# Optimization experiments

Measured on AMD Instinct MI355X. Metric: run time of the kernel, lower is better.

The kernel has to match this reference:

```python
import jax, jax.numpy as jnp
import numpy as np

N_NODES = 50000
N_EDGES = 800000
N_IN = 128
N_OPEN = 64
N_OUT = 40
N_LAYER = 4


def setup_inputs() -> dict:
    key = jax.random.key(0)
    ks = jax.random.split(key, 8)
    stdv, stdvp = 0.01, 1e-4
    KN1 = jnp.tile(jnp.eye(N_OPEN, dtype=jnp.float32)[None], (N_LAYER, 1, 1)) \
        + jax.random.uniform(ks[3], (N_LAYER, N_OPEN, N_OPEN), jnp.float32) * stdvp
    return {
        "xn": jax.random.normal(ks[0], (1, N_IN, N_NODES), jnp.float32),
        "K1Nopen": jax.random.normal(ks[1], (N_OPEN, N_IN), jnp.float32) * stdv,
        "KNclose": jax.random.normal(ks[2], (N_OUT, N_OPEN), jnp.float32) * stdv,
        "KN1": KN1,
        "att_src": 0.001 * jnp.ones((N_LAYER, 1, N_OPEN), jnp.float32),
        "att_dst": 0.001 * jnp.ones((N_LAYER, 1, N_OPEN), jnp.float32),
        "omega": jnp.ones((N_LAYER, N_OPEN), jnp.float32),
        "edge_i": jax.random.randint(ks[4], (N_EDGES,), 0, N_NODES, jnp.int32),
        "edge_j": jax.random.randint(ks[5], (N_EDGES,), 0, N_NODES, jnp.int32),
    }


def segment_softmax(logits, seg, num_segments):
    # numerically-stable softmax grouped by destination node (torch_geometric.utils.softmax)
    m = jax.ops.segment_max(logits, seg, num_segments=num_segments)
    e = jnp.exp(logits - m[seg])
    d = jax.ops.segment_sum(e, seg, num_segments=num_segments)
    return e / d[seg]


def reference(xn, K1Nopen, KNclose, KN1, att_src, att_dst, omega, edge_i, edge_j):
    N = xn.shape[-1]
    # gcn_norm(add_self_loops=True): augment edge list with self loops
    loops = jnp.arange(N, dtype=edge_i.dtype)
    I = jnp.concatenate([edge_i, loops])
    J = jnp.concatenate([edge_j, loops])

    # opening layer: 1x1 conv == matmul over channels, then relu
    x = jax.nn.relu(jnp.einsum('oc,bcn->bon', K1Nopen, xn))  # (1, nopen, N)

    for i in range(KN1.shape[0]):
        feat = x[0]  # (C, N), H=1 head
        # per-edge attention logits: a_src . x[:, I] + a_dst . x[:, J]
        a = att_src[i, 0] @ feat[:, I] + att_dst[i, 0] @ feat[:, J]  # (E,)
        a = jax.nn.leaky_relu(a, 0.2)
        W = segment_softmax(a, I, N)  # softmax over incoming edges of each node I
        # neighborNode: weighted gather of source features; neighborEdge: scatter-sum to dst
        msg = W[None, :] * feat[:, J]  # (C, E)
        spatial = jax.ops.segment_sum(msg.T, I, num_segments=N).T[None]  # (1, C, N)
        # omega residual mixing (per-channel)
        x = x - omega[i][None, :, None] * (x - spatial)
        # singleLayer openclose, act=False inside, relu outside
        x = jax.nn.relu(jnp.einsum('oc,bcn->bon', KN1[i], x))

    x = jnp.einsum('oc,bcn->bon', KNclose, x)  # (1, num_output, N)
    out = jax.nn.log_softmax(x[0].T, axis=-1)  # (N, num_output)
    return out
```

## Files before the change

### kernel.cpp

```cpp
#include <hip/hip_runtime.h>

#define NN 50000
#define NE 800000
#define NET 850000
#define OPEN_BLOCKS 782
#define EPB 1087
#define CAP 96

typedef unsigned int uint;
typedef unsigned short ushort;
typedef __attribute__((ext_vector_type(8))) short short8v;
typedef __attribute__((ext_vector_type(4))) float f32x4;

__device__ __forceinline__ float bcast_lane(float v, int l) {
    return __int_as_float(__builtin_amdgcn_readlane(__float_as_int(v), l));
}
__device__ __forceinline__ int ibcast(int v, int l) {
    return __builtin_amdgcn_readlane(v, l);
}
__device__ __forceinline__ float wred_max(float v) {
#pragma unroll
    for (int off = 32; off; off >>= 1) v = fmaxf(v, __shfl_xor(v, off, 64));
    return v;
}
__device__ __forceinline__ float wred_sum(float v) {
#pragma unroll
    for (int off = 32; off; off >>= 1) v += __shfl_xor(v, off, 64);
    return v;
}
__device__ __forceinline__ void wred_max2(float& a, float& b) {
#pragma unroll
    for (int off = 32; off; off >>= 1) {
        float ta = __shfl_xor(a, off, 64);
        float tb = __shfl_xor(b, off, 64);
        a = fmaxf(a, ta);
        b = fmaxf(b, tb);
    }
}
__device__ __forceinline__ void wred_sum2(float& a, float& b) {
#pragma unroll
    for (int off = 32; off; off >>= 1) {
        float ta = __shfl_xor(a, off, 64);
        float tb = __shfl_xor(b, off, 64);
        a += ta;
        b += tb;
    }
}
__device__ __forceinline__ ushort f2bf(float f) {
    uint u = __float_as_uint(f);
    return (ushort)((u + 0x7fffu + ((u >> 16) & 1u)) >> 16);
}
__device__ __forceinline__ float bflo(uint u) { return __uint_as_float(u << 16); }
__device__ __forceinline__ float bfhi(uint u) { return __uint_as_float(u & 0xffff0000u); }
__device__ __forceinline__ float lrelu(float a) { return (a > 0.f) ? a : 0.2f * a; }

__device__ __forceinline__ void acc8_fma(float* acc8, float wgt, uint4 v) {
    acc8[0] = fmaf(wgt, bflo(v.x), acc8[0]);
    acc8[1] = fmaf(wgt, bfhi(v.x), acc8[1]);
    acc8[2] = fmaf(wgt, bflo(v.y), acc8[2]);
    acc8[3] = fmaf(wgt, bfhi(v.y), acc8[3]);
    acc8[4] = fmaf(wgt, bflo(v.z), acc8[4]);
    acc8[5] = fmaf(wgt, bfhi(v.z), acc8[5]);
    acc8[6] = fmaf(wgt, bflo(v.w), acc8[6]);
    acc8[7] = fmaf(wgt, bfhi(v.w), acc8[7]);
}
__device__ __forceinline__ uint4 pack8(const float* v) {
    uint4 p;
    p.x = (uint)f2bf(v[0]) | ((uint)f2bf(v[1]) << 16);
    p.y = (uint)f2bf(v[2]) | ((uint)f2bf(v[3]) << 16);
    p.z = (uint)f2bf(v[4]) | ((uint)f2bf(v[5]) << 16);
    p.w = (uint)f2bf(v[6]) | ((uint)f2bf(v[7]) << 16);
    return p;
}

__device__ void node_aggregate_generic(const ushort* __restrict__ xin,
                                       const float* __restrict__ darr,
                                       const int* __restrict__ csrj,
                                       int rs, int deg, float s_n,
                                       int lane, int c8, float* out8) {
    float acc8[8] = {0.f, 0.f, 0.f, 0.f, 0.f, 0.f, 0.f, 0.f};
    int re = rs + deg;
    float mxd = -1e30f;
    for (int e = rs + lane; e < re; e += 64) mxd = fmaxf(mxd, darr[csrj[e]]);
    mxd = wred_max(mxd);
    float mx = lrelu(s_n + mxd);
    float sm = 0.f;
    for (int e = rs + lane; e < re; e += 64)
        sm += __expf(lrelu(s_n + darr[csrj[e]]) - mx);
    sm = wred_sum(sm);
    float inv = 1.f / sm;
    for (int e = rs; e < re; ++e) {
        int j = csrj[e];
        float w = __expf(lrelu(s_n + darr[j]) - mx);
        uint4 v = *(const uint4*)(xin + (((size_t)j) << 6) + (c8 << 3));
        acc8_fma(acc8, w, v);
    }
#pragma unroll
    for (int q = 0; q < 8; ++q) out8[q] = acc8[q] * inv;
}

__device__ __forceinline__ void dual_aggregate(const ushort* __restrict__ xin,
                                               const float* __restrict__ darr,
                                               const int* __restrict__ csrj,
                                               int r0, int deg0, float sn0, int jl0, float dl0,
                                               int r1, int deg1, float sn1, int jl1, float dl1,
                                               int lane, int g, int c8,
                                               float* o0, float* o1) {
    if (deg0 <= 64 && deg1 <= 64) {
        float m0 = dl0, m1 = dl1;
        wred_max2(m0, m1);
        float mx0 = lrelu(sn0 + m0);
        float mx1 = lrelu(sn1 + m1);
        float w0 = (lane < deg0) ? __expf(lrelu(sn0 + dl0) - mx0) : 0.f;
        float w1 = (lane < deg1) ? __expf(lrelu(sn1 + dl1) - mx1) : 0.f;
        float su0 = w0, su1 = w1;
        wred_sum2(su0, su1);
        float inv0 = 1.f / su0, inv1 = 1.f / su1;

        float acc0[8] = {0.f, 0.f, 0.f, 0.f, 0.f, 0.f, 0.f, 0.f};
        float acc1[8] = {0.f, 0.f, 0.f, 0.f, 0.f, 0.f, 0.f, 0.f};
        int md = min(deg0, deg1);
        int tt = 0;
        for (; tt + 16 <= md; tt += 16) {
            int e0 = tt + g, e1 = tt + 8 + g;
            int   ja = __shfl(jl0, e0); float wa = __shfl(w0, e0);
            int   jb = __shfl(jl0, e1); float wb = __shfl(w0, e1);
            int   jc = __shfl(jl1, e0); float wc = __shfl(w1, e0);
            int   jd = __shfl(jl1, e1); float wd = __shfl(w1, e1);
            uint4 va = *(const uint4*)(xin + (((size_t)ja) << 6) + (c8 << 3));
            uint4 vb = *(const uint4*)(xin + (((size_t)jb) << 6) + (c8 << 3));
            uint4 vc = *(const uint4*)(xin + (((size_t)jc) << 6) + (c8 << 3));
            uint4 vd = *(const uint4*)(xin + (((size_t)jd) << 6) + (c8 << 3));
            acc8_fma(acc0, wa, va);
            acc8_fma(acc0, wb, vb);
            acc8_fma(acc1, wc, vc);
            acc8_fma(acc1, wd, vd);
        }
        for (; tt + 8 <= md; tt += 8) {
            int e = tt + g;
            int   ja = __shfl(jl0, e); float wa = __shfl(w0, e);
            int   jc = __shfl(jl1, e); float wc = __shfl(w1, e);
            uint4 va = *(const uint4*)(xin + (((size_t)ja) << 6) + (c8 << 3));
            uint4 vc = *(const uint4*)(xin + (((size_t)jc) << 6) + (c8 << 3));
            acc8_fma(acc0, wa, va);
            acc8_fma(acc1, wc, vc);
        }
        for (int u = tt; u < deg0; u += 8) {
            int e = u + g;
            bool ok = e < deg0;
            int ec = ok ? e : 0;
            int   j = __shfl(jl0, ec);
            float w = ok ? __shfl(w0, ec) : 0.f;
            uint4 v = *(const uint4*)(xin + (((size_t)j) << 6) + (c8 << 3));
            acc8_fma(acc0, w, v);
        }
        for (int u = tt; u < deg1; u += 8) {
            int e = u + g;
            bool ok = e < deg1;
            int ec = ok ? e : 0;
            int   j = __shfl(jl1, ec);
            float w = ok ? __shfl(w1, ec) : 0.f;
            uint4 v = *(const uint4*)(xin + (((size_t)j) << 6) + (c8 << 3));
            acc8_fma(acc1, w, v);
        }
#pragma unroll
        for (int q = 0; q < 8; ++q) {
            float a = acc0[q], b = acc1[q];
            float ta = __shfl_xor(a, 8, 64),  tb = __shfl_xor(b, 8, 64);
            a += ta; b += tb;
            ta = __shfl_xor(a, 16, 64); tb = __shfl_xor(b, 16, 64);
            a += ta; b += tb;
            ta = __shfl_xor(a, 32, 64); tb = __shfl_xor(b, 32, 64);
            a += ta; b += tb;
            o0[q] = a * inv0;
            o1[q] = b * inv1;
        }
    } else {
        node_aggregate_generic(xin, darr, csrj, r0, deg0, sn0, lane, c8, o0);
        node_aggregate_generic(xin, darr, csrj, r1, deg1, sn1, lane, c8, o1);
    }
}

__device__ __forceinline__ void fill_edge(int* __restrict__ deg,
                                          int* __restrict__ csrj, int i, int j,
                                          int& slot_out, bool ok) {
    slot_out = ok ? atomicAdd(&deg[i], 1) : 0;
}

__device__ __forceinline__ void fill_phase(const int* __restrict__ ei,
                                           const int* __restrict__ ej,
                                           int* __restrict__ deg,
                                           int* __restrict__ csrj,
                                           int bid, int t) {
    int base = bid * EPB;
    int end = base + EPB;
    if (end > NET) end = NET;
    int e0 = base + t, e1 = e0 + 256, e2 = e0 + 512, e3 = e0 + 768, e4 = e0 + 1024;
    bool o0 = e0 < end, o1 = e1 < end, o2 = e2 < end, o3 = e3 < end, o4 = e4 < end;
    int i0 = 0, j0 = 0, i1 = 0, j1 = 0, i2 = 0, j2 = 0, i3 = 0, j3 = 0, i4 = 0, j4 = 0;
    if (o0) { if (e0 < NE) { i0 = ei[e0]; j0 = ej[e0]; } else { i0 = e0 - NE; j0 = i0; } }
    if (o1) { if (e1 < NE) { i1 = ei[e1]; j1 = ej[e1]; } else { i1 = e1 - NE; j1 = i1; } }
    if (o2) { if (e2 < NE) { i2 = ei[e2]; j2 = ej[e2]; } else { i2 = e2 - NE; j2 = i2; } }
    if (o3) { if (e3 < NE) { i3 = ei[e3]; j3 = ej[e3]; } else { i3 = e3 - NE; j3 = i3; } }
    if (o4) { if (e4 < NE) { i4 = ei[e4]; j4 = ej[e4]; } else { i4 = e4 - NE; j4 = i4; } }
    int p0 = 0, p1 = 0, p2 = 0, p3 = 0, p4 = 0;
    if (o0) p0 = atomicAdd(&deg[i0], 1);
    if (o1) p1 = atomicAdd(&deg[i1], 1);
    if (o2) p2 = atomicAdd(&deg[i2], 1);
    if (o3) p3 = atomicAdd(&deg[i3], 1);
    if (o4) p4 = atomicAdd(&deg[i4], 1);
    if (o0 && p0 < CAP) csrj[(size_t)i0 * CAP + p0] = j0;
    if (o1 && p1 < CAP) csrj[(size_t)i1 * CAP + p1] = j1;
    if (o2 && p2 < CAP) csrj[(size_t)i2 * CAP + p2] = j2;
    if (o3 && p3 < CAP) csrj[(size_t)i3 * CAP + p3] = j3;
    if (o4 && p4 < CAP) csrj[(size_t)i4 * CAP + p4] = j4;
}

__global__ __launch_bounds__(256) void k_openfill(const float* __restrict__ xn,
                                                  const float* __restrict__ K1,
                                                  const float* __restrict__ att_s,
                                                  const float* __restrict__ att_d,
                                                  ushort* __restrict__ x0,
                                                  float* __restrict__ s0,
                                                  float* __restrict__ d0,
                                                  const int* __restrict__ ei,
                                                  const int* __restrict__ ej,
                                                  int* __restrict__ deg,
                                                  int* __restrict__ csrj) {
    __shared__ float xs[64][65];
    __shared__ float Kt[64][65];
    int t = threadIdx.x;
    int bid = blockIdx.x;

    bool fill_first = (bid & 1);
    if (fill_first) fill_phase(ei, ej, deg, csrj, bid, t);

    int n0 = bid * 64;
    int tx = t & 15;
    int ty = t >> 4;
    float acc[4][4] = {};

    for (int half = 0; half < 2; ++half) {
        if (half) __syncthreads();
        for (int idx = t; idx < 4096; idx += 256) {
            int c = idx >> 6, o = idx & 63;
            Kt[c][o] = K1[o * 128 + half * 64 + c];
        }
        if (n0 + 64 <= NN) {
            for (int idx = t; idx < 1024; idx += 256) {
                int c = idx >> 4, l4 = (idx & 15) * 4;
                float4 v = *(const float4*)&xn[(size_t)(half * 64 + c) * NN + n0 + l4];
                *(float4*)&xs[c][l4] = v;
            }
        } else {
            for (int idx = t; idx < 4096; idx += 256) {
                int c = idx >> 6, ln = idx & 63;
                int n = n0 + ln;
                xs[c][ln] = (n < NN) ? xn[(size_t)(half * 64 + c) * NN + n] : 0.f;
            }
        }
        __syncthreads();

        for (int c = 0; c < 64; ++c) {
            float4 xv = *(const float4*)&xs[c][ty * 4];
            float4 kv = *(const float4*)&Kt[c][tx * 4];
            acc[0][0] = fmaf(xv.x, kv.x, acc[0][0]); acc[0][1] = fmaf(xv.x, kv.y, acc[0][1]);
            acc[0][2] = fmaf(xv.x, kv.z, acc[0][2]); acc[0][3] = fmaf(xv.x, kv.w, acc[0][3]);
            acc[1][0] = fmaf(xv.y, kv.x, acc[1][0]); acc[1][1] = fmaf(xv.y, kv.y, acc[1][1]);
            acc[1][2] = fmaf(xv.y, kv.z, acc[1][2]); acc[1][3] = fmaf(xv.y, kv.w, acc[1][3]);
            acc[2][0] = fmaf(xv.z, kv.x, acc[2][0]); acc[2][1] = fmaf(xv.z, kv.y, acc[2][1]);
            acc[2][2] = fmaf(xv.z, kv.z, acc[2][2]); acc[2][3] = fmaf(xv.z, kv.w, acc[2][3]);
            acc[3][0] = fmaf(xv.w, kv.x, acc[3][0]); acc[3][1] = fmaf(xv.w, kv.y, acc[3][1]);
            acc[3][2] = fmaf(xv.w, kv.z, acc[3][2]); acc[3][3] = fmaf(xv.w, kv.w, acc[3][3]);
        }
    }

    float asv[4], adv[4];
#pragma unroll
    for (int j = 0; j < 4; ++j) { asv[j] = att_s[tx * 4 + j]; adv[j] = att_d[tx * 4 + j]; }

#pragma unroll
    for (int i = 0; i < 4; ++i) {
        int n = n0 + ty * 4 + i;
        if (n < NN) {
            float4 r;
            r.x = fmaxf(acc[i][0], 0.f); r.y = fmaxf(acc[i][1], 0.f);
            r.z = fmaxf(acc[i][2], 0.f); r.w = fmaxf(acc[i][3], 0.f);
            float ps = r.x * asv[0] + r.y * asv[1] + r.z * asv[2] + r.w * asv[3];
            float pd = r.x * adv[0] + r.y * adv[1] + r.z * adv[2] + r.w * adv[3];
#pragma unroll
            for (int off = 1; off < 16; off <<= 1) {
                ps += __shfl_xor(ps, off, 64);
                pd += __shfl_xor(pd, off, 64);
            }
            if (tx == 0) { s0[n] = ps; d0[n] = pd; }
            ushort4 h;
            h.x = f2bf(r.x); h.y = f2bf(r.y); h.z = f2bf(r.z); h.w = f2bf(r.w);
            *(ushort4*)&x0[(size_t)n * 64 + tx * 4] = h;
        }
    }

    if (!fill_first) fill_phase(ei, ej, deg, csrj, bid, t);
}

template <int SD>
__global__ __launch_bounds__(256, 4) void k_layer(const ushort* __restrict__ xin,
                                                  ushort* __restrict__ xout,
                                                  const float* __restrict__ sarr,
                                                  const float* __restrict__ darr,
                                                  float* __restrict__ snext,
                                                  float* __restrict__ dnext,
                                                  const int* __restrict__ deg,
                                                  const int* __restrict__ csrj,
                                                  const float* __restrict__ Kl,
                                                  const float* __restrict__ om_l,
                                                  const float* __restrict__ atts_n,
                                                  const float* __restrict__ attd_n) {
    __shared__ ushort Tl[32][72];
    __shared__ ushort Kb[64][72];
    __shared__ float spart[32], dpart[32];

    int t = threadIdx.x;
    int lane = t & 63;
    int wid = t >> 6;
    int g = lane >> 3, c8 = lane & 7;

    for (int u = t; u < 512; u += 256) {
        int row = u >> 3, cb = (u & 7) * 8;
        float4 f0 = *(const float4*)&Kl[row * 64 + cb];
        float4 f1 = *(const float4*)&Kl[row * 64 + cb + 4];
        float v8[8] = {f0.x, f0.y, f0.z, f0.w, f1.x, f1.y, f1.z, f1.w};
        *(uint4*)&Kb[row][cb] = pack8(v8);
    }
    if (SD && t < 32) { spart[t] = 0.f; dpart[t] = 0.f; }

    float om8[8];
    {
        float4 a = *(const float4*)&om_l[c8 * 8];
        float4 b = *(const float4*)&om_l[c8 * 8 + 4];
        om8[0] = a.x; om8[1] = a.y; om8[2] = a.z; om8[3] = a.w;
        om8[4] = b.x; om8[5] = b.y; om8[6] = b.z; om8[7] = b.w;
    }

    int nblk = blockIdx.x * 32;
    int nw0 = nblk + wid * 8;

    int   dgv = ((lane < 8) && (nw0 + lane < NN)) ? deg[nw0 + lane] : 0;
    float snv = ((lane < 8) && (nw0 + lane < NN)) ? sarr[nw0 + lane] : 0.f;

    const uint4 zero4 = {0u, 0u, 0u, 0u};

    bool  c_v = (nw0 < NN);
    int   c_deg0 = min(ibcast(dgv, 0), CAP);
    int   c_deg1 = min(ibcast(dgv, 1), CAP);
    int   c_b0 = nw0 * CAP, c_b1 = (nw0 + 1) * CAP;
    float c_sn0 = bcast_lane(snv, 0), c_sn1 = bcast_lane(snv, 1);
    int   c_jl0 = (lane < c_deg0) ? csrj[c_b0 + lane] : 0;
    int   c_jl1 = (lane < c_deg1) ? csrj[c_b1 + lane] : 0;
    float c_dl0 = (lane < c_deg0) ? darr[c_jl0] : -1e30f;
    float c_dl1 = (lane < c_deg1) ? darr[c_jl1] : -1e30f;
    uint4 c_x0 = c_v ? *(const uint4*)(xin + (((size_t)nw0) << 6) + (c8 << 3)) : zero4;
    uint4 c_x1 = c_v ? *(const uint4*)(xin + (((size_t)(nw0 + 1)) << 6) + (c8 << 3)) : zero4;

#pragma unroll
    for (int rp = 0; rp < 4; ++rp) {
        int   nx_b0 = 0, nx_b1 = 0, nx_deg0 = 0, nx_deg1 = 0, nx_jl0 = 0, nx_jl1 = 0;
        float nx_sn0 = 0.f, nx_sn1 = 0.f, nx_dl0 = -1e30f, nx_dl1 = -1e30f;
        uint4 nx_x0 = zero4, nx_x1 = zero4;
        bool  nx_v = false;
        if (rp < 3) {
            int nn0 = nw0 + 2 * rp + 2;
            nx_v = (nn0 < NN);
            nx_deg0 = min(ibcast(dgv, 2 * rp + 2), CAP);
            nx_deg1 = min(ibcast(dgv, 2 * rp + 3), CAP);
            nx_b0 = nn0 * CAP;
            nx_b1 = (nn0 + 1) * CAP;
            nx_sn0 = bcast_lane(snv, 2 * rp + 2);
            nx_sn1 = bcast_lane(snv, 2 * rp + 3);
            nx_jl0 = (lane < nx_deg0) ? csrj[nx_b0 + lane] : 0;
            nx_jl1 = (lane < nx_deg1) ? csrj[nx_b1 + lane] : 0;
            nx_dl0 = (lane < nx_deg0) ? darr[nx_jl0] : -1e30f;
            nx_dl1 = (lane < nx_deg1) ? darr[nx_jl1] : -1e30f;
            if (nx_v) {
                nx_x0 = *(const uint4*)(xin + (((size_t)nn0) << 6) + (c8 << 3));
                nx_x1 = *(const uint4*)(xin + (((size_t)(nn0 + 1)) << 6) + (c8 << 3));
            }
        }

        if (c_v) {
            float t0a[8], t1a[8];
            dual_aggregate(xin, darr, csrj, c_b0, c_deg0, c_sn0, c_jl0, c_dl0,
                           c_b1, c_deg1, c_sn1, c_jl1, c_dl1, lane, g, c8, t0a, t1a);

            float xc;
            xc = bflo(c_x0.x); t0a[0] = xc - om8[0] * (xc - t0a[0]);
            xc = bfhi(c_x0.x); t0a[1] = xc - om8[1] * (xc - t0a[1]);
            xc = bflo(c_x0.y); t0a[2] = xc - om8[2] * (xc - t0a[2]);
            xc = bfhi(c_x0.y); t0a[3] = xc - om8[3] * (xc - t0a[3]);
            xc = bflo(c_x0.z); t0a[4] = xc - om8[4] * (xc - t0a[4]);
            xc = bfhi(c_x0.z); t0a[5] = xc - om8[5] * (xc - t0a[5]);
            xc = bflo(c_x0.w); t0a[6] = xc - om8[6] * (xc - t0a[6]);
            xc = bfhi(c_x0.w); t0a[7] = xc - om8[7] * (xc - t0a[7]);
            xc = bflo(c_x1.x); t1a[0] = xc - om8[0] * (xc - t1a[0]);
            xc = bfhi(c_x1.x); t1a[1] = xc - om8[1] * (xc - t1a[1]);
            xc = bflo(c_x1.y); t1a[2] = xc - om8[2] * (xc - t1a[2]);
            xc = bfhi(c_x1.y); t1a[3] = xc - om8[3] * (xc - t1a[3]);
            xc = bflo(c_x1.z); t1a[4] = xc - om8[4] * (xc - t1a[4]);
            xc = bfhi(c_x1.z); t1a[5] = xc - om8[5] * (xc - t1a[5]);
            xc = bflo(c_x1.w); t1a[6] = xc - om8[6] * (xc - t1a[6]);
            xc = bfhi(c_x1.w); t1a[7] = xc - om8[7] * (xc - t1a[7]);

            int lr = wid * 8 + 2 * rp;
            if (g == 0) {
                *(uint4*)&Tl[lr][c8 * 8] = pack8(t0a);
            } else if (g == 1) {
                *(uint4*)&Tl[lr + 1][c8 * 8] = pack8(t1a);
            }
        }

        c_b0 = nx_b0; c_b1 = nx_b1; c_v = nx_v;
        c_deg0 = nx_deg0; c_deg1 = nx_deg1;
        c_sn0 = nx_sn0; c_sn1 = nx_sn1;
        c_jl0 = nx_jl0; c_jl1 = nx_jl1;
        c_dl0 = nx_dl0; c_dl1 = nx_dl1;
        c_x0 = nx_x0; c_x1 = nx_x1;
    }
    __syncthreads();

    {
        int mt = wid >> 1;
        int arow = mt * 16 + (lane & 15);
        int koff = (lane >> 4) * 8;
        short8v a0 = *(const short8v*)&Tl[arow][koff];
        short8v a1 = *(const short8v*)&Tl[arow][32 + koff];
        int col0 = (wid & 1) * 32 + (lane & 15);
        int col1 = col0 + 16;
        short8v b00 = *(const short8v*)&Kb[col0][koff];
        short8v b01 = *(const short8v*)&Kb[col0][32 + koff];
        short8v b10 = *(const short8v*)&Kb[col1][koff];
        short8v b11 = *(const short8v*)&Kb[col1][32 + koff];
        f32x4 acc0 = {0.f, 0.f, 0.f, 0.f};
        f32x4 acc1 = {0.f, 0.f, 0.f, 0.f};
        acc0 = __builtin_amdgcn_mfma_f32_16x16x32_bf16(a0, b00, acc0, 0, 0, 0);
        acc0 = __builtin_amdgcn_mfma_f32_16x16x32_bf16(a1, b01, acc0, 0, 0, 0);
        acc1 = __builtin_amdgcn_mfma_f32_16x16x32_bf16(a0, b10, acc1, 0, 0, 0);
        acc1 = __builtin_amdgcn_mfma_f32_16x16x32_bf16(a1, b11, acc1, 0, 0, 0);

        float as0 = 0.f, ad0 = 0.f, as1 = 0.f, ad1 = 0.f;
        if (SD) {
            as0 = atts_n[col0]; ad0 = attd_n[col0];
            as1 = atts_n[col1]; ad1 = attd_n[col1];
        }

        int rbase = mt * 16 + (lane >> 4) * 4;
#pragma unroll
        for (int i = 0; i < 4; ++i) {
            int row = rbase + i;
            int n = nblk + row;
            bool valid = (n < NN);
            float y0 = fmaxf(acc0[i], 0.f);
            float y1 = fmaxf(acc1[i], 0.f);
            if (valid) {
                xout[(size_t)n * 64 + col0] = f2bf(y0);
                xout[(size_t)n * 64 + col1] = f2bf(y1);
            }
            if (SD) {
                float ps = as0 * y0 + as1 * y1;
                float pd = ad0 * y0 + ad1 * y1;
#pragma unroll
                for (int m = 1; m < 16; m <<= 1) {
                    ps += __shfl_xor(ps, m, 64);
                    pd += __shfl_xor(pd, m, 64);
                }
                if ((lane & 15) == 0 && valid) {
                    atomicAdd(&spart[row], ps);
                    atomicAdd(&dpart[row], pd);
                }
            }
        }
    }

    if (SD) {
        __syncthreads();
        if (t < 32) {
            int n = nblk + t;
            if (n < NN) { snext[n] = spart[t]; dnext[n] = dpart[t]; }
        }
    }
}

__global__ __launch_bounds__(512) void k_close(const ushort* __restrict__ xin,
                                               const float* __restrict__ KNc,
                                               float* __restrict__ out) {
    __shared__ float Kpad[40][65];
    int t = threadIdx.x;
    for (int idx = t; idx < 40 * 64; idx += 512)
        Kpad[idx >> 6][idx & 63] = KNc[idx];
    __syncthreads();

    int lane = t & 63;
    int wid = t >> 6;
    int kr = (lane < 40) ? lane : 0;
    int base = (blockIdx.x * 8 + wid) * 4;

#pragma unroll
    for (int p = 0; p < 2; ++p) {
        int n0 = base + p * 2;
        if (n0 >= NN) break;

        float xv0 = bflo((uint)xin[(size_t)n0 * 64 + lane]);
        float xv1 = bflo((uint)xin[(size_t)(n0 + 1) * 64 + lane]);

        float z0a = 0.f, z0b = 0.f, z1a = 0.f, z1b = 0.f;
#pragma unroll
        for (int c = 0; c < 64; c += 2) {
            float k0 = (lane < 40) ? Kpad[kr][c] : 0.f;
            float k1 = (lane < 40) ? Kpad[kr][c + 1] : 0.f;
            float b0 = bcast_lane(xv0, c), b1 = bcast_lane(xv0, c + 1);
            float c0 = bcast_lane(xv1, c), c1 = bcast_lane(xv1, c + 1);
            z0a = fmaf(k0, b0, z0a);
            z0b = fmaf(k1, b1, z0b);
            z1a = fmaf(k0, c0, z1a);
            z1b = fmaf(k1, c1, z1b);
        }
        float z0 = z0a + z0b;
        float z1 = z1a + z1b;

        float zm0 = (lane < 40) ? z0 : -1e30f;
        float zm1 = (lane < 40) ? z1 : -1e30f;
        wred_max2(zm0, zm1);
        float p0 = (lane < 40) ? __expf(z0 - zm0) : 0.f;
        float p1 = (lane < 40) ? __expf(z1 - zm1) : 0.f;
        wred_sum2(p0, p1);
        if (lane < 40) {
            out[(size_t)n0 * 40 + lane] = z0 - zm0 - logf(p0);
            out[(size_t)(n0 + 1) * 40 + lane] = z1 - zm1 - logf(p1);
        }
    }
}

extern "C" void kernel_launch(void* const* d_in, const int* in_sizes, int n_in,
                              void* d_out, int out_size, void* d_ws, size_t ws_size,
                              hipStream_t stream) {
    const float* xn    = (const float*)d_in[0];
    const float* K1    = (const float*)d_in[1];
    const float* KNc   = (const float*)d_in[2];
    const float* KN1   = (const float*)d_in[3];
    const float* atts  = (const float*)d_in[4];
    const float* attd  = (const float*)d_in[5];
    const float* omega = (const float*)d_in[6];
    const int*   ei    = (const int*)d_in[7];
    const int*   ej    = (const int*)d_in[8];
    float* out = (float*)d_out;

    char* ws = (char*)d_ws;
    size_t off = 0;
    auto alloc = [&](size_t b) -> void* {
        void* p = ws + off;
        off = (off + b + 255) & ~(size_t)255;
        return p;
    };
    ushort* xa    = (ushort*)alloc((size_t)NN * 64 * 2);
    ushort* xb    = (ushort*)alloc((size_t)NN * 64 * 2);
    float* sA     = (float*)alloc((size_t)NN * 4);
    float* dA     = (float*)alloc((size_t)NN * 4);
    float* sB     = (float*)alloc((size_t)NN * 4);
    float* dB     = (float*)alloc((size_t)NN * 4);
    int*   deg    = (int*)alloc((size_t)NN * 4);
    int*   csrj   = (int*)alloc((size_t)NN * CAP * 4);
    if (off > ws_size) return;

    (void)hipMemsetAsync(deg, 0, (size_t)NN * 4, stream);
    k_openfill<<<OPEN_BLOCKS, 256, 0, stream>>>(xn, K1, atts, attd, xa, sA, dA,
                                                ei, ej, deg, csrj);

    const int LBLK = (NN + 31) / 32;
    const ushort* xi = xa; ushort* xo = xb;
    const float* si = sA; const float* di = dA;
    float* so = sB; float* dn = dB;
    for (int l = 0; l < 3; ++l) {
        k_layer<1><<<LBLK, 256, 0, stream>>>(xi, xo, si, di, so, dn, deg, csrj,
                                             KN1 + (size_t)l * 4096, omega + l * 64,
                                             atts + (size_t)(l + 1) * 64,
                                             attd + (size_t)(l + 1) * 64);
        const ushort* t0 = xi; xi = xo; xo = (ushort*)t0;
        const float* t1 = si; si = so; so = (float*)t1;
        const float* t2 = di; di = dn; dn = (float*)t2;
    }
    k_layer<0><<<LBLK, 256, 0, stream>>>(xi, xo, si, di, so, dn, deg, csrj,
                                         KN1 + (size_t)3 * 4096, omega + 3 * 64,
                                         atts, attd);

    k_close<<<(NN + 31) / 32, 512, 0, stream>>>(xo, KNc, out);
}
```

Before: 265.2 us.

## Store CSR neighbor indices as 16-bit and shrink layer blocks to 16 nodes

Neighbor indices in the padded CSR are stored as ushort instead of int, which halves index storage and the bytes read per edge in every layer. This is valid only because the node count fits in 16 bits. The layer kernel now handles 16 nodes per block, with four nodes per wave and one MFMA column tile per wave, and its launch bound is raised to 8 blocks per CU for higher occupancy. Bounds checks are dropped because the node count divides evenly by 16, so the kernel now depends on that fixed problem size.

```diff
diff --git a/kernel.cpp b/kernel.cpp
--- a/kernel.cpp
+++ b/kernel.cpp
@@ -75,7 +75,7 @@
 
 __device__ void node_aggregate_generic(const ushort* __restrict__ xin,
                                        const float* __restrict__ darr,
-                                       const int* __restrict__ csrj,
+                                       const ushort* __restrict__ csrj,
                                        int rs, int deg, float s_n,
                                        int lane, int c8, float* out8) {
     float acc8[8] = {0.f, 0.f, 0.f, 0.f, 0.f, 0.f, 0.f, 0.f};
@@ -101,7 +101,7 @@
 
 __device__ __forceinline__ void dual_aggregate(const ushort* __restrict__ xin,
                                                const float* __restrict__ darr,
-                                               const int* __restrict__ csrj,
+                                               const ushort* __restrict__ csrj,
                                                int r0, int deg0, float sn0, int jl0, float dl0,
                                                int r1, int deg1, float sn1, int jl1, float dl1,
                                                int lane, int g, int c8,
@@ -181,16 +181,10 @@
     }
 }
 
-__device__ __forceinline__ void fill_edge(int* __restrict__ deg,
-                                          int* __restrict__ csrj, int i, int j,
-                                          int& slot_out, bool ok) {
-    slot_out = ok ? atomicAdd(&deg[i], 1) : 0;
-}
-
 __device__ __forceinline__ void fill_phase(const int* __restrict__ ei,
                                            const int* __restrict__ ej,
                                            int* __restrict__ deg,
-                                           int* __restrict__ csrj,
+                                           ushort* __restrict__ csrj,
                                            int bid, int t) {
     int base = bid * EPB;
     int end = base + EPB;
@@ -209,11 +203,11 @@
     if (o2) p2 = atomicAdd(&deg[i2], 1);
     if (o3) p3 = atomicAdd(&deg[i3], 1);
     if (o4) p4 = atomicAdd(&deg[i4], 1);
-    if (o0 && p0 < CAP) csrj[(size_t)i0 * CAP + p0] = j0;
-    if (o1 && p1 < CAP) csrj[(size_t)i1 * CAP + p1] = j1;
-    if (o2 && p2 < CAP) csrj[(size_t)i2 * CAP + p2] = j2;
-    if (o3 && p3 < CAP) csrj[(size_t)i3 * CAP + p3] = j3;
-    if (o4 && p4 < CAP) csrj[(size_t)i4 * CAP + p4] = j4;
+    if (o0 && p0 < CAP) csrj[(size_t)i0 * CAP + p0] = (ushort)j0;
+    if (o1 && p1 < CAP) csrj[(size_t)i1 * CAP + p1] = (ushort)j1;
+    if (o2 && p2 < CAP) csrj[(size_t)i2 * CAP + p2] = (ushort)j2;
+    if (o3 && p3 < CAP) csrj[(size_t)i3 * CAP + p3] = (ushort)j3;
+    if (o4 && p4 < CAP) csrj[(size_t)i4 * CAP + p4] = (ushort)j4;
 }
 
 __global__ __launch_bounds__(256) void k_openfill(const float* __restrict__ xn,
@@ -226,7 +220,7 @@
                                                   const int* __restrict__ ei,
                                                   const int* __restrict__ ej,
                                                   int* __restrict__ deg,
-                                                  int* __restrict__ csrj) {
+                                                  ushort* __restrict__ csrj) {
     __shared__ float xs[64][65];
     __shared__ float Kt[64][65];
     int t = threadIdx.x;
@@ -304,21 +298,21 @@
 }
 
 template <int SD>
-__global__ __launch_bounds__(256, 4) void k_layer(const ushort* __restrict__ xin,
+__global__ __launch_bounds__(256, 8) void k_layer(const ushort* __restrict__ xin,
                                                   ushort* __restrict__ xout,
                                                   const float* __restrict__ sarr,
                                                   const float* __restrict__ darr,
                                                   float* __restrict__ snext,
                                                   float* __restrict__ dnext,
                                                   const int* __restrict__ deg,
-                                                  const int* __restrict__ csrj,
+                                                  const ushort* __restrict__ csrj,
                                                   const float* __restrict__ Kl,
                                                   const float* __restrict__ om_l,
                                                   const float* __restrict__ atts_n,
                                                   const float* __restrict__ attd_n) {
-    __shared__ ushort Tl[32][72];
+    __shared__ ushort Tl[16][72];
     __shared__ ushort Kb[64][72];
-    __shared__ float spart[32], dpart[32];
+    __shared__ float spart[16], dpart[16];
 
     int t = threadIdx.x;
     int lane = t & 63;
@@ -332,7 +326,7 @@
         float v8[8] = {f0.x, f0.y, f0.z, f0.w, f1.x, f1.y, f1.z, f1.w};
         *(uint4*)&Kb[row][cb] = pack8(v8);
     }
-    if (SD && t < 32) { spart[t] = 0.f; dpart[t] = 0.f; }
+    if (SD && t < 16) { spart[t] = 0.f; dpart[t] = 0.f; }
 
     float om8[8];
     {
@@ -342,15 +336,12 @@
         om8[4] = b.x; om8[5] = b.y; om8[6] = b.z; om8[7] = b.w;
     }
 
-    int nblk = blockIdx.x * 32;
-    int nw0 = nblk + wid * 8;
-
-    int   dgv = ((lane < 8) && (nw0 + lane < NN)) ? deg[nw0 + lane] : 0;
-    float snv = ((lane < 8) && (nw0 + lane < NN)) ? sarr[nw0 + lane] : 0.f;
-
-    const uint4 zero4 = {0u, 0u, 0u, 0u};
-
-    bool  c_v = (nw0 < NN);
+    int nblk = blockIdx.x * 16;
+    int nw0 = nblk + wid * 4;
+
+    int   dgv = (lane < 4) ? deg[nw0 + lane] : 0;
+    float snv = (lane < 4) ? sarr[nw0 + lane] : 0.f;
+
     int   c_deg0 = min(ibcast(dgv, 0), CAP);
     int   c_deg1 = min(ibcast(dgv, 1), CAP);
     int   c_b0 = nw0 * CAP, c_b1 = (nw0 + 1) * CAP;
@@ -359,35 +350,31 @@
     int   c_jl1 = (lane < c_deg1) ? csrj[c_b1 + lane] : 0;
     float c_dl0 = (lane < c_deg0) ? darr[c_jl0] : -1e30f;
     float c_dl1 = (lane < c_deg1) ? darr[c_jl1] : -1e30f;
-    uint4 c_x0 = c_v ? *(const uint4*)(xin + (((size_t)nw0) << 6) + (c8 << 3)) : zero4;
-    uint4 c_x1 = c_v ? *(const uint4*)(xin + (((size_t)(nw0 + 1)) << 6) + (c8 << 3)) : zero4;
-
-#pragma unroll
-    for (int rp = 0; rp < 4; ++rp) {
+    uint4 c_x0 = *(const uint4*)(xin + (((size_t)nw0) << 6) + (c8 << 3));
+    uint4 c_x1 = *(const uint4*)(xin + (((size_t)(nw0 + 1)) << 6) + (c8 << 3));
+
+#pragma unroll
+    for (int rp = 0; rp < 2; ++rp) {
         int   nx_b0 = 0, nx_b1 = 0, nx_deg0 = 0, nx_deg1 = 0, nx_jl0 = 0, nx_jl1 = 0;
         float nx_sn0 = 0.f, nx_sn1 = 0.f, nx_dl0 = -1e30f, nx_dl1 = -1e30f;
-        uint4 nx_x0 = zero4, nx_x1 = zero4;
-        bool  nx_v = false;
-        if (rp < 3) {
-            int nn0 = nw0 + 2 * rp + 2;
-            nx_v = (nn0 < NN);
-            nx_deg0 = min(ibcast(dgv, 2 * rp + 2), CAP);
-            nx_deg1 = min(ibcast(dgv, 2 * rp + 3), CAP);
+        uint4 nx_x0, nx_x1;
+        if (rp < 1) {
+            int nn0 = nw0 + 2;
+            nx_deg0 = min(ibcast(dgv, 2), CAP);
+            nx_deg1 = min(ibcast(dgv, 3), CAP);
             nx_b0 = nn0 * CAP;
             nx_b1 = (nn0 + 1) * CAP;
-            nx_sn0 = bcast_lane(snv, 2 * rp + 2);
-            nx_sn1 = bcast_lane(snv, 2 * rp + 3);
+            nx_sn0 = bcast_lane(snv, 2);
+            nx_sn1 = bcast_lane(snv, 3);
             nx_jl0 = (lane < nx_deg0) ? csrj[nx_b0 + lane] : 0;
             nx_jl1 = (lane < nx_deg1) ? csrj[nx_b1 + lane] : 0;
             nx_dl0 = (lane < nx_deg0) ? darr[nx_jl0] : -1e30f;
             nx_dl1 = (lane < nx_deg1) ? darr[nx_jl1] : -1e30f;
-            if (nx_v) {
-                nx_x0 = *(const uint4*)(xin + (((size_t)nn0) << 6) + (c8 << 3));
-                nx_x1 = *(const uint4*)(xin + (((size_t)(nn0 + 1)) << 6) + (c8 << 3));
-            }
-        }
-
-        if (c_v) {
+            nx_x0 = *(const uint4*)(xin + (((size_t)nn0) << 6) + (c8 << 3));
+            nx_x1 = *(const uint4*)(xin + (((size_t)(nn0 + 1)) << 6) + (c8 << 3));
+        }
+
+        {
             float t0a[8], t1a[8];
             dual_aggregate(xin, darr, csrj, c_b0, c_deg0, c_sn0, c_jl0, c_dl0,
                            c_b1, c_deg1, c_sn1, c_jl1, c_dl1, lane, g, c8, t0a, t1a);
@@ -410,7 +397,7 @@
             xc = bflo(c_x1.w); t1a[6] = xc - om8[6] * (xc - t1a[6]);
             xc = bfhi(c_x1.w); t1a[7] = xc - om8[7] * (xc - t1a[7]);
 
-            int lr = wid * 8 + 2 * rp;
+            int lr = wid * 4 + 2 * rp;
             if (g == 0) {
                 *(uint4*)&Tl[lr][c8 * 8] = pack8(t0a);
             } else if (g == 1) {
@@ -418,7 +405,7 @@
             }
         }
 
-        c_b0 = nx_b0; c_b1 = nx_b1; c_v = nx_v;
+        c_b0 = nx_b0; c_b1 = nx_b1;
         c_deg0 = nx_deg0; c_deg1 = nx_deg1;
         c_sn0 = nx_sn0; c_sn1 = nx_sn1;
         c_jl0 = nx_jl0; c_jl1 = nx_jl1;
@@ -428,51 +415,36 @@
     __syncthreads();
 
     {
-        int mt = wid >> 1;
-        int arow = mt * 16 + (lane & 15);
+        int arow = lane & 15;
         int koff = (lane >> 4) * 8;
         short8v a0 = *(const short8v*)&Tl[arow][koff];
         short8v a1 = *(const short8v*)&Tl[arow][32 + koff];
-        int col0 = (wid & 1) * 32 + (lane & 15);
-        int col1 = col0 + 16;
-        short8v b00 = *(const short8v*)&Kb[col0][koff];
-        short8v b01 = *(const short8v*)&Kb[col0][32 + koff];
-        short8v b10 = *(const short8v*)&Kb[col1][koff];
-        short8v b11 = *(const short8v*)&Kb[col1][32 + koff];
-        f32x4 acc0 = {0.f, 0.f, 0.f, 0.f};
-        f32x4 acc1 = {0.f, 0.f, 0.f, 0.f};
-        acc0 = __builtin_amdgcn_mfma_f32_16x16x32_bf16(a0, b00, acc0, 0, 0, 0);
-        acc0 = __builtin_amdgcn_mfma_f32_16x16x32_bf16(a1, b01, acc0, 0, 0, 0);
-        acc1 = __builtin_amdgcn_mfma_f32_16x16x32_bf16(a0, b10, acc1, 0, 0, 0);
-        acc1 = __builtin_amdgcn_mfma_f32_16x16x32_bf16(a1, b11, acc1, 0, 0, 0);
-
-        float as0 = 0.f, ad0 = 0.f, as1 = 0.f, ad1 = 0.f;
-        if (SD) {
-            as0 = atts_n[col0]; ad0 = attd_n[col0];
-            as1 = atts_n[col1]; ad1 = attd_n[col1];
-        }
-
-        int rbase = mt * 16 + (lane >> 4) * 4;
+        int col = wid * 16 + (lane & 15);
+        short8v b0 = *(const short8v*)&Kb[col][koff];
+        short8v b1 = *(const short8v*)&Kb[col][32 + koff];
+        f32x4 acc = {0.f, 0.f, 0.f, 0.f};
+        acc = __builtin_amdgcn_mfma_f32_16x16x32_bf16(a0, b0, acc, 0, 0, 0);
+        acc = __builtin_amdgcn_mfma_f32_16x16x32_bf16(a1, b1, acc, 0, 0, 0);
+
+        float as_ = 0.f, ad_ = 0.f;
+        if (SD) { as_ = atts_n[col]; ad_ = attd_n[col]; }
+
+        int rbase = (lane >> 4) * 4;
 #pragma unroll
         for (int i = 0; i < 4; ++i) {
             int row = rbase + i;
             int n = nblk + row;
-            bool valid = (n < NN);
-            float y0 = fmaxf(acc0[i], 0.f);
-            float y1 = fmaxf(acc1[i], 0.f);
-            if (valid) {
-                xout[(size_t)n * 64 + col0] = f2bf(y0);
-                xout[(size_t)n * 64 + col1] = f2bf(y1);
-            }
+            float y = fmaxf(acc[i], 0.f);
+            xout[(size_t)n * 64 + col] = f2bf(y);
             if (SD) {
-                float ps = as0 * y0 + as1 * y1;
-                float pd = ad0 * y0 + ad1 * y1;
+                float ps = as_ * y;
+                float pd = ad_ * y;
 #pragma unroll
                 for (int m = 1; m < 16; m <<= 1) {
                     ps += __shfl_xor(ps, m, 64);
                     pd += __shfl_xor(pd, m, 64);
                 }
-                if ((lane & 15) == 0 && valid) {
+                if ((lane & 15) == 0) {
                     atomicAdd(&spart[row], ps);
                     atomicAdd(&dpart[row], pd);
                 }
@@ -482,9 +454,10 @@
 
     if (SD) {
         __syncthreads();
-        if (t < 32) {
+        if (t < 16) {
             int n = nblk + t;
-            if (n < NN) { snext[n] = spart[t]; dnext[n] = dpart[t]; }
+            snext[n] = spart[t];
+            dnext[n] = dpart[t];
         }
     }
 }
@@ -566,15 +539,15 @@
     float* dA     = (float*)alloc((size_t)NN * 4);
     float* sB     = (float*)alloc((size_t)NN * 4);
     float* dB     = (float*)alloc((size_t)NN * 4);
-    int*   deg    = (int*)alloc((size_t)NN * 4);
-    int*   csrj   = (int*)alloc((size_t)NN * CAP * 4);
+    int*    deg   = (int*)alloc((size_t)NN * 4);
+    ushort* csrj  = (ushort*)alloc((size_t)NN * CAP * 2);
     if (off > ws_size) return;
 
     (void)hipMemsetAsync(deg, 0, (size_t)NN * 4, stream);
     k_openfill<<<OPEN_BLOCKS, 256, 0, stream>>>(xn, K1, atts, attd, xa, sA, dA,
                                                 ei, ej, deg, csrj);
 
-    const int LBLK = (NN + 31) / 32;
+    const int LBLK = NN / 16;
     const ushort* xi = xa; ushort* xo = xb;
     const float* si = sA; const float* di = dA;
     float* so = sB; float* dn = dB;
```

Result: slower. 317.0 us (+19.6%).
